# Optimization experiments

Hardware: AMD Instinct MI355X
Metric: run time of the kernel (lower is better)

## Reference

```python
import jax, jax.numpy as jnp
import numpy as np

N, F = 8192, 512
RATIO = 0.5
K_KEEP = int(np.ceil(RATIO * N))  # segment_top_k with a single graph -> ceil(ratio*N)


def setup_inputs() -> dict:
    key = jax.random.key(0)
    k1, k2, k3 = jax.random.split(key, 3)
    X = jax.random.normal(k1, (N, F), dtype=jnp.float32)
    # sparse binary adjacency stored dense (single-mode TopKPool path)
    A = (jax.random.uniform(k2, (N, N)) < 0.005).astype(jnp.float32)
    kernel = jax.random.normal(k3, (F, 1), dtype=jnp.float32)
    return {"X": X, "A": A, "kernel": kernel}


def reference(X, A, kernel):
    # y = X p / ||p||  (scores, shape (N,1))
    p = kernel / jnp.linalg.norm(kernel)
    y = X @ p
    # i = rank(y, K): indices of top-K scores, sorted ascending
    _, idx = jax.lax.top_k(y[:, 0], K_KEEP)
    idx = jnp.sort(idx)
    # X' = (X * tanh(y))_i   (tanh gating; sigmoid_gating=False)
    features = X * jnp.tanh(y)
    X_pooled = jnp.take(features, idx, axis=0)          # (K, F)
    # A' = A_{i,i}
    A_pooled = jnp.take(jnp.take(A, idx, axis=0), idx, axis=1)  # (K, K)
    return X_pooled, A_pooled
```

## Files before the change

### kernel.cpp

```cpp
#include <hip/hip_runtime.h>
#include <math.h>

#define N 8192
#define F 512
#define KKEEP 4096

__global__ void scores_kernel(const float* __restrict__ X,
                              const float* __restrict__ kern,
                              unsigned long long* __restrict__ keys,
                              float* __restrict__ g,
                              int* __restrict__ rank) {
    int wave = threadIdx.x >> 6;
    int lane = threadIdx.x & 63;
    int row  = blockIdx.x * 4 + wave;
    if (row >= N) return;

    const float4* xr = (const float4*)(X + (size_t)row * F);
    const float4* kr = (const float4*)kern;

    float4 x0 = xr[lane * 2];
    float4 x1 = xr[lane * 2 + 1];
    float4 k0 = kr[lane * 2];
    float4 k1 = kr[lane * 2 + 1];

    double d = (double)x0.x * (double)k0.x + (double)x0.y * (double)k0.y +
               (double)x0.z * (double)k0.z + (double)x0.w * (double)k0.w +
               (double)x1.x * (double)k1.x + (double)x1.y * (double)k1.y +
               (double)x1.z * (double)k1.z + (double)x1.w * (double)k1.w;
    double s = (double)k0.x * (double)k0.x + (double)k0.y * (double)k0.y +
               (double)k0.z * (double)k0.z + (double)k0.w * (double)k0.w +
               (double)k1.x * (double)k1.x + (double)k1.y * (double)k1.y +
               (double)k1.z * (double)k1.z + (double)k1.w * (double)k1.w;

    #pragma unroll
    for (int off = 32; off > 0; off >>= 1) {
        d += __shfl_down(d, off);
        s += __shfl_down(s, off);
    }

    if (lane == 0) {
        float yn = (float)(d / sqrt(s));
        g[row] = tanhf(yn);
        rank[row] = 0;
        float yf = (float)d;
        unsigned int u  = __float_as_uint(yf);
        unsigned int ob = (u & 0x80000000u) ? ~u : (u | 0x80000000u);
        keys[row] = ((unsigned long long)ob << 32) |
                    (unsigned long long)(unsigned)(N - 1 - row);
    }
}

__global__ void rank_kernel(const unsigned long long* __restrict__ keys,
                            int* __restrict__ rank) {
    __shared__ unsigned long long sk[256];
    int t = threadIdx.x;
    sk[t] = keys[blockIdx.y * 256 + t];
    __syncthreads();

    int i = blockIdx.x * 256 + t;
    unsigned long long ki = keys[i];
    int cnt = 0;
    #pragma unroll 8
    for (int j = 0; j < 256; ++j)
        cnt += (sk[j] > ki) ? 1 : 0;
    atomicAdd(&rank[i], cnt);
}

__global__ void compact_kernel(const int* __restrict__ rank,
                               int* __restrict__ idx) {
    __shared__ int cnts[256];
    __shared__ int offs[256];
    int t = threadIdx.x;
    int base = t * 32;
    int c = 0;
    for (int u = 0; u < 32; ++u)
        c += (rank[base + u] < KKEEP) ? 1 : 0;
    cnts[t] = c;
    __syncthreads();
    if (t == 0) {
        int acc = 0;
        for (int u = 0; u < 256; ++u) { offs[u] = acc; acc += cnts[u]; }
    }
    __syncthreads();
    int pos = offs[t];
    for (int u = 0; u < 32; ++u) {
        int i = base + u;
        if (rank[i] < KKEEP) idx[pos++] = i;
    }
}

__global__ void xpool_kernel(const float* __restrict__ X,
                             const float* __restrict__ g,
                             const int* __restrict__ idx,
                             float* __restrict__ out) {
    int m = blockIdx.x;
    int row = idx[m];
    float gv = g[row];
    const float4* xr = (const float4*)(X + (size_t)row * F);
    float4* o = (float4*)(out + (size_t)m * F);
    float4 v = xr[threadIdx.x];
    v.x *= gv; v.y *= gv; v.z *= gv; v.w *= gv;
    o[threadIdx.x] = v;
}

__global__ void apool_kernel(const float* __restrict__ A,
                             const int* __restrict__ idx,
                             float* __restrict__ out) {
    __shared__ float srow[N];
    int m = blockIdx.x;
    int t = threadIdx.x;
    size_t row = (size_t)idx[m];
    const float4* ar4 = (const float4*)(A + row * (size_t)N);
    float4* sr4 = (float4*)srow;
    #pragma unroll
    for (int it = 0; it < 8; ++it)
        sr4[it * 256 + t] = ar4[it * 256 + t];
    __syncthreads();

    float* o = out + (size_t)m * KKEEP;
    #pragma unroll
    for (int it = 0; it < 4; ++it) {
        int n0 = (it * 256 + t) * 4;
        float4 v;
        v.x = srow[idx[n0 + 0]];
        v.y = srow[idx[n0 + 1]];
        v.z = srow[idx[n0 + 2]];
        v.w = srow[idx[n0 + 3]];
        *(float4*)(o + n0) = v;
    }
}

extern "C" void kernel_launch(void* const* d_in, const int* in_sizes, int n_in,
                              void* d_out, int out_size, void* d_ws, size_t ws_size,
                              hipStream_t stream) {
    const float* X    = (const float*)d_in[0];
    const float* A    = (const float*)d_in[1];
    const float* kern = (const float*)d_in[2];

    float* outX = (float*)d_out;
    float* outA = outX + (size_t)KKEEP * F;

    char* ws = (char*)d_ws;
    unsigned long long* keys = (unsigned long long*)ws;
    float* g   = (float*)(ws + 65536);
    int* rank  = (int*)(ws + 65536 + 32768);
    int* idx   = (int*)(ws + 65536 + 32768 + 32768);

    scores_kernel<<<N / 4, 256, 0, stream>>>(X, kern, keys, g, rank);
    rank_kernel<<<dim3(N / 256, N / 256), 256, 0, stream>>>(keys, rank);
    compact_kernel<<<1, 256, 0, stream>>>(rank, idx);
    xpool_kernel<<<KKEEP, 128, 0, stream>>>(X, g, idx, outX);
    apool_kernel<<<KKEEP, 256, 0, stream>>>(A, idx, outA);
}
```

Measured before the change: 380.1 us.

## Replace all-pairs rank counting with single-block histogram radix top-k selection

Drops the O(N^2) pairwise rank kernel and the serial compaction kernel, and adds one 1024-thread block. That block histograms the top 13 key bits, finds the threshold bucket by suffix scan, and ranks only the candidates in that bucket. It then compacts the selected indices in order with a prefix scan. This removes two launches and the pairwise comparison work, but runs selection on a single CU, and a crowded threshold bucket is capped at 2048 candidates.

```diff
diff --git a/kernel.cpp b/kernel.cpp
--- a/kernel.cpp
+++ b/kernel.cpp
@@ -8,8 +8,7 @@
 __global__ void scores_kernel(const float* __restrict__ X,
                               const float* __restrict__ kern,
                               unsigned long long* __restrict__ keys,
-                              float* __restrict__ g,
-                              int* __restrict__ rank) {
+                              float* __restrict__ g) {
     int wave = threadIdx.x >> 6;
     int lane = threadIdx.x & 63;
     int row  = blockIdx.x * 4 + wave;
@@ -41,7 +40,6 @@
     if (lane == 0) {
         float yn = (float)(d / sqrt(s));
         g[row] = tanhf(yn);
-        rank[row] = 0;
         float yf = (float)d;
         unsigned int u  = __float_as_uint(yf);
         unsigned int ob = (u & 0x80000000u) ? ~u : (u | 0x80000000u);
@@ -50,42 +48,104 @@
     }
 }
 
-__global__ void rank_kernel(const unsigned long long* __restrict__ keys,
-                            int* __restrict__ rank) {
-    __shared__ unsigned long long sk[256];
+#define NBUCK 8192
+#define CANDMAX 2048
+
+__global__ void __launch_bounds__(1024)
+select_kernel(const unsigned long long* __restrict__ keys,
+              int* __restrict__ idx) {
+    __shared__ int hist[NBUCK];
+    __shared__ int part[1024];
+    __shared__ unsigned long long cand[CANDMAX];
+    __shared__ int ncand, Tsh, rsh;
+
     int t = threadIdx.x;
-    sk[t] = keys[blockIdx.y * 256 + t];
-    __syncthreads();
-
-    int i = blockIdx.x * 256 + t;
-    unsigned long long ki = keys[i];
-    int cnt = 0;
-    #pragma unroll 8
-    for (int j = 0; j < 256; ++j)
-        cnt += (sk[j] > ki) ? 1 : 0;
-    atomicAdd(&rank[i], cnt);
-}
-
-__global__ void compact_kernel(const int* __restrict__ rank,
-                               int* __restrict__ idx) {
-    __shared__ int cnts[256];
-    __shared__ int offs[256];
-    int t = threadIdx.x;
-    int base = t * 32;
+
+    #pragma unroll
+    for (int u = 0; u < 8; ++u) hist[t + 1024 * u] = 0;
+    if (t == 0) ncand = 0;
+    __syncthreads();
+
+    unsigned long long k[8];
+    #pragma unroll
+    for (int u = 0; u < 8; ++u) {
+        k[u] = keys[t * 8 + u];
+        atomicAdd(&hist[(int)(k[u] >> 51)], 1);
+    }
+    __syncthreads();
+
     int c = 0;
-    for (int u = 0; u < 32; ++u)
-        c += (rank[base + u] < KKEEP) ? 1 : 0;
-    cnts[t] = c;
-    __syncthreads();
-    if (t == 0) {
-        int acc = 0;
-        for (int u = 0; u < 256; ++u) { offs[u] = acc; acc += cnts[u]; }
-    }
-    __syncthreads();
-    int pos = offs[t];
-    for (int u = 0; u < 32; ++u) {
-        int i = base + u;
-        if (rank[i] < KKEEP) idx[pos++] = i;
+    #pragma unroll
+    for (int u = 0; u < 8; ++u) c += hist[t * 8 + u];
+    part[t] = c;
+    __syncthreads();
+
+    for (int d = 1; d < 1024; d <<= 1) {
+        int v = part[t];
+        int w = (t + d < 1024) ? part[t + d] : 0;
+        __syncthreads();
+        part[t] = v + w;
+        __syncthreads();
+    }
+
+    {
+        int running = (t + 1 < 1024) ? part[t + 1] : 0;
+        #pragma unroll
+        for (int u = 7; u >= 0; --u) {
+            int b = t * 8 + u;
+            int h = hist[b];
+            if (running < KKEEP && running + h >= KKEEP) {
+                Tsh = b;
+                rsh = KKEEP - running;
+            }
+            running += h;
+        }
+    }
+    __syncthreads();
+    int T = Tsh, r = rsh, nc;
+
+    #pragma unroll
+    for (int u = 0; u < 8; ++u) {
+        if ((int)(k[u] >> 51) == T) {
+            int p = atomicAdd(&ncand, 1);
+            if (p < CANDMAX) cand[p] = k[u];
+        }
+    }
+    __syncthreads();
+    nc = ncand;
+    if (nc > CANDMAX) nc = CANDMAX;
+
+    #pragma unroll
+    for (int u = 0; u < 8; ++u) {
+        int b = (int)(k[u] >> 51);
+        int sel = 0;
+        if (b > T) sel = 1;
+        else if (b == T) {
+            int gt = 0;
+            for (int q = 0; q < nc; ++q) gt += (cand[q] > k[u]) ? 1 : 0;
+            sel = (gt < r) ? 1 : 0;
+        }
+        hist[t * 8 + u] = sel;
+    }
+    __syncthreads();
+
+    c = 0;
+    #pragma unroll
+    for (int u = 0; u < 8; ++u) c += hist[t * 8 + u];
+    part[t] = c;
+    __syncthreads();
+    for (int d = 1; d < 1024; d <<= 1) {
+        int v = part[t];
+        int w = (t >= d) ? part[t - d] : 0;
+        __syncthreads();
+        part[t] = v + w;
+        __syncthreads();
+    }
+    int off = (t > 0) ? part[t - 1] : 0;
+    #pragma unroll
+    for (int u = 0; u < 8; ++u) {
+        int i = t * 8 + u;
+        if (hist[i]) idx[off++] = i;
     }
 }
 
@@ -143,12 +203,10 @@
     char* ws = (char*)d_ws;
     unsigned long long* keys = (unsigned long long*)ws;
     float* g   = (float*)(ws + 65536);
-    int* rank  = (int*)(ws + 65536 + 32768);
-    int* idx   = (int*)(ws + 65536 + 32768 + 32768);
-
-    scores_kernel<<<N / 4, 256, 0, stream>>>(X, kern, keys, g, rank);
-    rank_kernel<<<dim3(N / 256, N / 256), 256, 0, stream>>>(keys, rank);
-    compact_kernel<<<1, 256, 0, stream>>>(rank, idx);
+    int* idx   = (int*)(ws + 65536 + 32768);
+
+    scores_kernel<<<N / 4, 256, 0, stream>>>(X, kern, keys, g);
+    select_kernel<<<1, 1024, 0, stream>>>(keys, idx);
     xpool_kernel<<<KKEEP, 128, 0, stream>>>(X, g, idx, outX);
     apool_kernel<<<KKEEP, 256, 0, stream>>>(A, idx, outA);
 }
```

After: 371.5 us. 2.3% less time.
